# Performance work log

Hardware: AMD Instinct MI355X
Metric: run time of the kernel (lower is better)

The kernel has to match this reference:

```python
import jax, jax.numpy as jnp
import numpy as np

D_MODEL = 1024
D_FF = 2048
N_EXPERTS = 4
TOP_K = 2
INIT_STD = 0.02


def setup_inputs() -> dict:
    key = jax.random.key(0)
    ks = jax.random.split(key, 5)
    hidden_states = jax.random.normal(ks[0], (2, 2048, D_MODEL), dtype=jnp.float32)
    # gate: nn.Linear(d_model, num_experts, bias=False) -> weight [E, D]
    w_gate = jax.random.normal(ks[1], (N_EXPERTS, D_MODEL), dtype=jnp.float32) * INIT_STD
    # per-expert GLU MLP weights, stacked over the expert axis
    w_gate_proj = jax.random.normal(ks[2], (N_EXPERTS, D_MODEL, D_FF), dtype=jnp.float32) * INIT_STD
    w_up_proj = jax.random.normal(ks[3], (N_EXPERTS, D_MODEL, D_FF), dtype=jnp.float32) * INIT_STD
    w_down_proj = jax.random.normal(ks[4], (N_EXPERTS, D_FF, D_MODEL), dtype=jnp.float32) * INIT_STD
    return {
        "hidden_states": hidden_states,
        "w_gate": w_gate,
        "w_gate_proj": w_gate_proj,
        "w_up_proj": w_up_proj,
        "w_down_proj": w_down_proj,
    }


def reference(hidden_states, w_gate, w_gate_proj, w_up_proj, w_down_proj):
    B, S, D = hidden_states.shape
    x = hidden_states.reshape(-1, D)  # [T, D]
    # --- routing ---
    router_logits = x @ w_gate.T  # [T, E]
    routing_probs = jax.nn.softmax(router_logits.astype(jnp.float32), axis=-1)
    topw, sel = jax.lax.top_k(routing_probs, TOP_K)  # [T, K]
    topw = topw / jnp.sum(topw, axis=-1, keepdims=True)  # norm_topk_prob=True
    topw = topw.astype(x.dtype)
    # combine weights per (token, expert): zero for non-selected experts
    cw = jnp.sum(jax.nn.one_hot(sel, N_EXPERTS, dtype=x.dtype) * topw[..., None], axis=1)  # [T, E]
    # --- expert GLU MLPs (dense over experts, masked combine) ---
    g = jnp.einsum('td,edf->etf', x, w_gate_proj)  # [E, T, F]
    u = jnp.einsum('td,edf->etf', x, w_up_proj)
    h = jax.nn.gelu(g, approximate=False) * u  # torch F.gelu default = exact erf
    y = jnp.einsum('etf,efd->etd', h, w_down_proj)  # [E, T, D]
    out = jnp.einsum('etd,te->td', y, cw)  # weighted scatter-combine
    # dropout p=0.0 (eval) -> identity
    return out.reshape(B, S, D)
```

## Files before the change

kernel.cpp:

```cpp
#include <hip/hip_runtime.h>
#include <hip/hip_bf16.h>
#include <math.h>


typedef float  f32x4 __attribute__((ext_vector_type(4)));
typedef short  s16x8 __attribute__((ext_vector_type(8)));

__device__ __forceinline__ unsigned short f2bf(float f) {
  union { float f; unsigned int u; } v; v.f = f;
  return (unsigned short)((v.u + 0x7fffu + ((v.u >> 16) & 1u)) >> 16);
}

__device__ __forceinline__ void glds16(const void* g, void* l) {
  __builtin_amdgcn_global_load_lds(
      (const __attribute__((address_space(1))) void*)g,
      (__attribute__((address_space(3))) void*)l, 16, 0, 0);
}

__global__ void k_routing(const float* __restrict__ x, const float* __restrict__ wg,
                          float* __restrict__ cw, int* __restrict__ idx,
                          int* __restrict__ cnt, unsigned short* __restrict__ Xb) {
  const int lane = threadIdx.x & 63;
  const int tok  = blockIdx.x * 4 + (threadIdx.x >> 6);
  const float4* X4 = (const float4*)x + (size_t)tok * 256;
  const float4* W4 = (const float4*)wg;
  ushort4* O4 = (ushort4*)Xb + (size_t)tok * 256;
  float a0 = 0.f, a1 = 0.f, a2 = 0.f, a3 = 0.f;
#pragma unroll
  for (int j = 0; j < 4; ++j) {
    const int d4 = j * 64 + lane;
    const float4 v = X4[d4];
    ushort4 o;
    o.x = f2bf(v.x); o.y = f2bf(v.y); o.z = f2bf(v.z); o.w = f2bf(v.w);
    O4[d4] = o;
    float4 w;
    w = W4[0 * 256 + d4]; a0 += v.x * w.x + v.y * w.y + v.z * w.z + v.w * w.w;
    w = W4[1 * 256 + d4]; a1 += v.x * w.x + v.y * w.y + v.z * w.z + v.w * w.w;
    w = W4[2 * 256 + d4]; a2 += v.x * w.x + v.y * w.y + v.z * w.z + v.w * w.w;
    w = W4[3 * 256 + d4]; a3 += v.x * w.x + v.y * w.y + v.z * w.z + v.w * w.w;
  }
#pragma unroll
  for (int off = 32; off; off >>= 1) {
    a0 += __shfl_xor(a0, off);
    a1 += __shfl_xor(a1, off);
    a2 += __shfl_xor(a2, off);
    a3 += __shfl_xor(a3, off);
  }
  if (lane == 0) {
    float l[4] = {a0, a1, a2, a3};
    const float m = fmaxf(fmaxf(l[0], l[1]), fmaxf(l[2], l[3]));
    float p[4];
#pragma unroll
    for (int e = 0; e < 4; ++e) p[e] = expf(l[e] - m);
    int i1 = 0; float b1 = p[0];
#pragma unroll
    for (int e = 1; e < 4; ++e) if (p[e] > b1) { b1 = p[e]; i1 = e; }
    int i2 = -1; float b2 = -1.f;
#pragma unroll
    for (int e = 0; e < 4; ++e) if (e != i1 && p[e] > b2) { b2 = p[e]; i2 = e; }
    const float inv = 1.f / (b1 + b2);
    float o[4] = {0.f, 0.f, 0.f, 0.f};
    o[i1] = b1 * inv; o[i2] = b2 * inv;
    *(float4*)(cw + (size_t)tok * 4) = make_float4(o[0], o[1], o[2], o[3]);
    const int p1 = atomicAdd(&cnt[i1], 1); idx[i1 * 4096 + p1] = tok;
    const int p2 = atomicAdd(&cnt[i2], 1); idx[i2 * 4096 + p2] = tok;
  }
}

__global__ void k_offsets(const int* __restrict__ cnt, int* __restrict__ off) {
  if (threadIdx.x == 0 && blockIdx.x == 0) {
    int o = 0, q = 0, p = 0;
#pragma unroll
    for (int e = 0; e < 4; ++e) {
      off[e] = o; off[4 + e] = q; off[9 + e] = p;
      o += (cnt[e] + 255) & ~255;
      q += (cnt[e] + 255) >> 8;
      p += (cnt[e] + 127) >> 7;
    }
    off[8] = q; off[13] = p;
  }
}

__global__ void k_tcvt_all(const float* __restrict__ wgp, const float* __restrict__ wup,
                           const float* __restrict__ wdp,
                           unsigned short* __restrict__ Wcat,
                           unsigned short* __restrict__ Wdt) {
  __shared__ float t[64][65];
  const int z = blockIdx.z;
  const int tx = threadIdx.x, ty = threadIdx.y;
  const float* in; unsigned short* outp; int R, C, c0, r0, cat = 0, addup = 0;
  if (z < 8) {
    R = 1024; C = 2048;
    const int e = z & 3;
    in   = (z < 4 ? wgp : wup) + (size_t)e * 1024 * 2048;
    outp = Wcat + (size_t)e * 4096 * 1024;
    c0 = blockIdx.x * 64; r0 = blockIdx.y * 64;
    cat = 1; addup = (z >= 4) ? 16 : 0;
  } else {
    R = 2048; C = 1024;
    const int e = z & 3;
    in   = wdp + (size_t)e * 2048 * 1024;
    outp = Wdt + (size_t)e * 2048 * 1024;
    c0 = blockIdx.y * 64; r0 = blockIdx.x * 64;
  }
#pragma unroll
  for (int i = 0; i < 16; ++i) {
    const int r = i * 4 + ty;
    t[r][tx] = in[(size_t)(r0 + r) * C + c0 + tx];
  }
  __syncthreads();
#pragma unroll
  for (int i = 0; i < 16; ++i) {
    const int cc = i * 4 + ty;
    const int f = c0 + cc;
    const int orow = cat ? (((f >> 4) << 5) + (f & 15) + addup) : f;
    outp[(size_t)orow * R + r0 + tx] = f2bf(t[tx][cc]);
  }
}

__global__ __launch_bounds__(512, 2)
void k_gemm1(const unsigned short* __restrict__ Xb,
             const unsigned short* __restrict__ Wcat,
             unsigned short* __restrict__ H,
             const int* __restrict__ idx, const int* __restrict__ cnt,
             const int* __restrict__ off) {
  const int w0 = (blockIdx.x & 7) * 72 + (blockIdx.x >> 3);
  const int bn = w0 / 36, mt = w0 % 36;
  const int* t1 = off + 4;
  if (mt >= t1[4]) return;
  const int e = (mt >= t1[1]) + (mt >= t1[2]) + (mt >= t1[3]);
  const int local = mt - t1[e];
  const int cn = cnt[e];
  const int lr0 = local * 256;
  const int hrow0 = off[e] + lr0;

  __shared__ __align__(16) unsigned short lds[2][2][256 * 64];

  const int tid = threadIdx.x;
  const int lane = tid & 63, wv = tid >> 6;
  const int wm = wv >> 2, wn = wv & 3;
  const int l15 = lane & 15;
  const int kb0 = ((lane >> 4) * 16) ^ ((lane & 7) << 4);
  const int kb1 = kb0 ^ 64;
  const int lrow = lane >> 3;
  const int scol = ((lane & 7) ^ lrow) * 8;
  const int wbase = wv * 8;

  int tk[4];
#pragma unroll
  for (int j = 0; j < 4; ++j)
    tk[j] = idx[e * 4096 + min(lr0 + j * 64 + wbase + lrow, cn - 1)];

  const unsigned short* Wb = Wcat + (size_t)e * 4096 * 1024 + (size_t)(bn * 256) * 1024;

  f32x4 acc[8][4] = {};

#pragma unroll
  for (int j = 0; j < 4; ++j)
    glds16(Xb + (size_t)tk[j] * 1024 + scol, &lds[0][0][(j * 64 + wbase) * 64]);
#pragma unroll
  for (int j = 0; j < 4; ++j)
    glds16(Wb + (size_t)(j * 64 + wbase + lrow) * 1024 + scol, &lds[0][1][(j * 64 + wbase) * 64]);

  for (int kt = 0; kt < 16; ++kt) {
    const int cur = kt & 1;
    asm volatile("s_waitcnt vmcnt(0)" ::: "memory");
    asm volatile("s_barrier" ::: "memory");
    if (kt < 15) {
      const int ko = (kt + 1) * 64;
#pragma unroll
      for (int j = 0; j < 4; ++j)
        glds16(Xb + (size_t)tk[j] * 1024 + ko + scol, &lds[cur ^ 1][0][(j * 64 + wbase) * 64]);
#pragma unroll
      for (int j = 0; j < 4; ++j)
        glds16(Wb + (size_t)(j * 64 + wbase + lrow) * 1024 + ko + scol, &lds[cur ^ 1][1][(j * 64 + wbase) * 64]);
    }
    const char* Ab = (const char*)lds[cur][0];
    const char* Bb = (const char*)lds[cur][1];
    s16x8 bfr[4][2];
#pragma unroll
    for (int ni = 0; ni < 4; ++ni) {
      const int row = wn * 64 + ni * 16 + l15;
      bfr[ni][0] = *(const s16x8*)(Bb + row * 128 + kb0);
      bfr[ni][1] = *(const s16x8*)(Bb + row * 128 + kb1);
    }
#pragma unroll
    for (int p = 0; p < 4; ++p) {
      const int r0a = wm * 128 + (2 * p) * 16 + l15;
      const int r1a = wm * 128 + (2 * p + 1) * 16 + l15;
      const s16x8 a0k0 = *(const s16x8*)(Ab + r0a * 128 + kb0);
      const s16x8 a0k1 = *(const s16x8*)(Ab + r0a * 128 + kb1);
      const s16x8 a1k0 = *(const s16x8*)(Ab + r1a * 128 + kb0);
      const s16x8 a1k1 = *(const s16x8*)(Ab + r1a * 128 + kb1);
      __builtin_amdgcn_s_setprio(1);
#pragma unroll
      for (int ni = 0; ni < 4; ++ni) {
        acc[2 * p][ni]     = __builtin_amdgcn_mfma_f32_16x16x32_bf16(a0k0, bfr[ni][0], acc[2 * p][ni], 0, 0, 0);
        acc[2 * p][ni]     = __builtin_amdgcn_mfma_f32_16x16x32_bf16(a0k1, bfr[ni][1], acc[2 * p][ni], 0, 0, 0);
        acc[2 * p + 1][ni] = __builtin_amdgcn_mfma_f32_16x16x32_bf16(a1k0, bfr[ni][0], acc[2 * p + 1][ni], 0, 0, 0);
        acc[2 * p + 1][ni] = __builtin_amdgcn_mfma_f32_16x16x32_bf16(a1k1, bfr[ni][1], acc[2 * p + 1][ni], 0, 0, 0);
      }
      __builtin_amdgcn_s_setprio(0);
    }
  }

  const int rbase = hrow0 + wm * 128;
#pragma unroll
  for (int mi = 0; mi < 8; ++mi)
#pragma unroll
    for (int q = 0; q < 2; ++q)
#pragma unroll
      for (int r = 0; r < 4; ++r) {
        const int row = rbase + mi * 16 + (lane >> 4) * 4 + r;
        const int col = bn * 128 + wn * 32 + q * 16 + l15;
        const float g = acc[mi][2 * q][r];
        const float u = acc[mi][2 * q + 1][r];
        const float h = 0.5f * g * (1.0f + erff(g * 0.70710678118654752f)) * u;
        H[(size_t)row * 2048 + col] = f2bf(h);
      }
}

__global__ __launch_bounds__(256, 2)
void k_gemm2(const unsigned short* __restrict__ H,
             const unsigned short* __restrict__ Wdt,
             const float* __restrict__ cw,
             const int* __restrict__ idx, const int* __restrict__ cnt,
             const int* __restrict__ off,
             float* __restrict__ out) {
  const int w = (blockIdx.x & 7) * 68 + (blockIdx.x >> 3);
  const int mt = w >> 3, bn = w & 7;
  const int* t2 = off + 9;
  if (mt >= t2[4]) return;
  const int e = (mt >= t2[1]) + (mt >= t2[2]) + (mt >= t2[3]);
  const int local = mt - t2[e];
  const int cn = cnt[e];
  const int lr0 = local * 128;
  const int hrow0 = off[e] + lr0;

  __shared__ __align__(16) unsigned short sA[128 * 64];
  __shared__ __align__(16) unsigned short sB[128 * 64];
  const int tid = threadIdx.x;
  const int lane = tid & 63, wid = tid >> 6;
  const int wm = wid >> 1, wn = wid & 1;
  const int srow = lane >> 3;
  const int scol = (lane & 7) * 8;

  const unsigned short* Ha = H + (size_t)hrow0 * 2048;
  const unsigned short* Wd = Wdt + (size_t)e * 1024 * 2048 + (size_t)(bn * 128) * 2048;

  f32x4 acc[4][4] = {};

  for (int kt = 0; kt < 32; ++kt) {
    const int k0 = kt * 64;
#pragma unroll
    for (int i = 0; i < 4; ++i) {
      const int c = wid * 4 + i;
      const int row = c * 8 + srow;
      glds16(Ha + (size_t)row * 2048 + k0 + scol, &sA[c * 512]);
      glds16(Wd + (size_t)row * 2048 + k0 + scol, &sB[c * 512]);
    }
    __syncthreads();
#pragma unroll
    for (int ks = 0; ks < 2; ++ks) {
      const int ko = ks * 32 + (lane >> 4) * 8;
      s16x8 a[4], b[4];
#pragma unroll
      for (int mi = 0; mi < 4; ++mi)
        a[mi] = *(const s16x8*)&sA[(wm * 64 + mi * 16 + (lane & 15)) * 64 + ko];
#pragma unroll
      for (int ni = 0; ni < 4; ++ni)
        b[ni] = *(const s16x8*)&sB[(wn * 64 + ni * 16 + (lane & 15)) * 64 + ko];
#pragma unroll
      for (int mi = 0; mi < 4; ++mi)
#pragma unroll
        for (int ni = 0; ni < 4; ++ni)
          acc[mi][ni] = __builtin_amdgcn_mfma_f32_16x16x32_bf16(a[mi], b[ni], acc[mi][ni], 0, 0, 0);
    }
    __syncthreads();
  }
#pragma unroll
  for (int mi = 0; mi < 4; ++mi)
#pragma unroll
    for (int r = 0; r < 4; ++r) {
      const int lr = lr0 + wm * 64 + mi * 16 + (lane >> 4) * 4 + r;
      if (lr < cn) {
        const int tok = idx[e * 4096 + lr];
        const float wgt = cw[(size_t)tok * 4 + e];
        float* orow = out + (size_t)tok * 1024 + bn * 128 + wn * 64 + (lane & 15);
#pragma unroll
        for (int ni = 0; ni < 4; ++ni)
          atomicAdd(orow + ni * 16, acc[mi][ni][r] * wgt);
      }
    }
}

extern "C" void kernel_launch(void* const* d_in, const int* in_sizes, int n_in,
                              void* d_out, int out_size, void* d_ws, size_t ws_size,
                              hipStream_t stream) {
  const float* x     = (const float*)d_in[0];
  const float* wgate = (const float*)d_in[1];
  const float* wgp   = (const float*)d_in[2];
  const float* wup   = (const float*)d_in[3];
  const float* wdp   = (const float*)d_in[4];
  float* out = (float*)d_out;

  char* ws = (char*)d_ws;
  float* cw            = (float*)ws;
  int*   idx           = (int*)(ws + 65536);
  int*   cnt           = (int*)(ws + 131072);
  int*   off           = (int*)(ws + 131136);
  unsigned short* Xb   = (unsigned short*)(ws + 131584);
  unsigned short* Wcat = Xb   + (size_t)4096 * 1024;
  unsigned short* Wdt  = Wcat + (size_t)4 * 4096 * 1024;
  unsigned short* H    = Wdt  + (size_t)4 * 1024 * 2048;

  hipMemsetAsync(cnt, 0, 16, stream);
  hipMemsetAsync(out, 0, (size_t)4096 * 1024 * 4, stream);
  k_routing<<<1024, 256, 0, stream>>>(x, wgate, cw, idx, cnt, Xb);
  k_offsets<<<1, 64, 0, stream>>>(cnt, off);
  k_tcvt_all<<<dim3(32, 16, 12), dim3(64, 4), 0, stream>>>(wgp, wup, wdp, Wcat, Wdt);

  k_gemm1<<<576, 512, 0, stream>>>(Xb, Wcat, H, idx, cnt, off);
  k_gemm2<<<544, 256, 0, stream>>>(H, Wdt, cw, idx, cnt, off, out);
}
```

Measured before the change: 314.0 us.

## Double-buffer LDS in down-projection GEMM with XOR swizzle and prefetch

The down-projection GEMM kernel now uses two LDS buffers, prefetching the next K tile via global_load_lds while MFMAs run on the current one, with a single barrier per iteration instead of two. LDS rows are XOR-swizzled on both the write and read side to avoid bank conflicts on the fragment loads. s_setprio is raised around MFMA bursts. This doubles LDS use to 64KB per block, which may limit occupancy under launch_bounds(256,2).

```diff
diff --git a/kernel.cpp b/kernel.cpp
--- a/kernel.cpp
+++ b/kernel.cpp
@@ -237,47 +237,66 @@
   const int lr0 = local * 128;
   const int hrow0 = off[e] + lr0;
 
-  __shared__ __align__(16) unsigned short sA[128 * 64];
-  __shared__ __align__(16) unsigned short sB[128 * 64];
-  const int tid = threadIdx.x;
-  const int lane = tid & 63, wid = tid >> 6;
+  __shared__ __align__(16) unsigned short lds[2][2][128 * 64];
+
+  const int lane = threadIdx.x & 63, wid = threadIdx.x >> 6;
   const int wm = wid >> 1, wn = wid & 1;
-  const int srow = lane >> 3;
-  const int scol = (lane & 7) * 8;
+  const int l15 = lane & 15;
+  const int kb0 = ((lane >> 4) * 16) ^ ((lane & 7) << 4);
+  const int kb1 = kb0 ^ 64;
+  const int lrow = lane >> 3;
+  const int scol = ((lane & 7) ^ lrow) * 8;
+  const int wbase = wid * 8;
 
   const unsigned short* Ha = H + (size_t)hrow0 * 2048;
   const unsigned short* Wd = Wdt + (size_t)e * 1024 * 2048 + (size_t)(bn * 128) * 2048;
 
   f32x4 acc[4][4] = {};
 
+#pragma unroll
+  for (int j = 0; j < 4; ++j) {
+    const int r = j * 32 + wbase;
+    glds16(Ha + (size_t)(r + lrow) * 2048 + scol, &lds[0][0][r * 64]);
+    glds16(Wd + (size_t)(r + lrow) * 2048 + scol, &lds[0][1][r * 64]);
+  }
+
   for (int kt = 0; kt < 32; ++kt) {
-    const int k0 = kt * 64;
-#pragma unroll
-    for (int i = 0; i < 4; ++i) {
-      const int c = wid * 4 + i;
-      const int row = c * 8 + srow;
-      glds16(Ha + (size_t)row * 2048 + k0 + scol, &sA[c * 512]);
-      glds16(Wd + (size_t)row * 2048 + k0 + scol, &sB[c * 512]);
-    }
-    __syncthreads();
-#pragma unroll
-    for (int ks = 0; ks < 2; ++ks) {
-      const int ko = ks * 32 + (lane >> 4) * 8;
-      s16x8 a[4], b[4];
-#pragma unroll
-      for (int mi = 0; mi < 4; ++mi)
-        a[mi] = *(const s16x8*)&sA[(wm * 64 + mi * 16 + (lane & 15)) * 64 + ko];
-#pragma unroll
-      for (int ni = 0; ni < 4; ++ni)
-        b[ni] = *(const s16x8*)&sB[(wn * 64 + ni * 16 + (lane & 15)) * 64 + ko];
-#pragma unroll
-      for (int mi = 0; mi < 4; ++mi)
-#pragma unroll
-        for (int ni = 0; ni < 4; ++ni)
-          acc[mi][ni] = __builtin_amdgcn_mfma_f32_16x16x32_bf16(a[mi], b[ni], acc[mi][ni], 0, 0, 0);
-    }
-    __syncthreads();
-  }
+    const int cur = kt & 1;
+    asm volatile("s_waitcnt vmcnt(0)" ::: "memory");
+    asm volatile("s_barrier" ::: "memory");
+    if (kt < 31) {
+      const int ko = (kt + 1) * 64;
+#pragma unroll
+      for (int j = 0; j < 4; ++j) {
+        const int r = j * 32 + wbase;
+        glds16(Ha + (size_t)(r + lrow) * 2048 + ko + scol, &lds[cur ^ 1][0][r * 64]);
+        glds16(Wd + (size_t)(r + lrow) * 2048 + ko + scol, &lds[cur ^ 1][1][r * 64]);
+      }
+    }
+    const char* Ab = (const char*)lds[cur][0];
+    const char* Bb = (const char*)lds[cur][1];
+    s16x8 bfr[4][2];
+#pragma unroll
+    for (int ni = 0; ni < 4; ++ni) {
+      const int row = wn * 64 + ni * 16 + l15;
+      bfr[ni][0] = *(const s16x8*)(Bb + row * 128 + kb0);
+      bfr[ni][1] = *(const s16x8*)(Bb + row * 128 + kb1);
+    }
+#pragma unroll
+    for (int mi = 0; mi < 4; ++mi) {
+      const int ra = wm * 64 + mi * 16 + l15;
+      const s16x8 ak0 = *(const s16x8*)(Ab + ra * 128 + kb0);
+      const s16x8 ak1 = *(const s16x8*)(Ab + ra * 128 + kb1);
+      __builtin_amdgcn_s_setprio(1);
+#pragma unroll
+      for (int ni = 0; ni < 4; ++ni) {
+        acc[mi][ni] = __builtin_amdgcn_mfma_f32_16x16x32_bf16(ak0, bfr[ni][0], acc[mi][ni], 0, 0, 0);
+        acc[mi][ni] = __builtin_amdgcn_mfma_f32_16x16x32_bf16(ak1, bfr[ni][1], acc[mi][ni], 0, 0, 0);
+      }
+      __builtin_amdgcn_s_setprio(0);
+    }
+  }
+
 #pragma unroll
   for (int mi = 0; mi < 4; ++mi)
 #pragma unroll
@@ -286,7 +305,7 @@
       if (lr < cn) {
         const int tok = idx[e * 4096 + lr];
         const float wgt = cw[(size_t)tok * 4 + e];
-        float* orow = out + (size_t)tok * 1024 + bn * 128 + wn * 64 + (lane & 15);
+        float* orow = out + (size_t)tok * 1024 + bn * 128 + wn * 64 + l15;
 #pragma unroll
         for (int ni = 0; ni < 4; ++ni)
           atomicAdd(orow + ni * 16, acc[mi][ni][r] * wgt);
```

Result: no change. 315.2 us (+0.4%).
